# Performance work log

Measured on AMD Instinct MI355X. Metric: run time of the kernel, lower is better.

Reference implementation:

```python
import jax, jax.numpy as jnp
import numpy as np

B, S, H = 2, 1024, 2048
E_ROUTED = 8
E = E_ROUTED + 1          # +1 unconditional expert
I_MOE = 1408
I_SHARED = 5632
TOP_K = 2
UNCOND_LABEL = 1000
EPS = 1e-12


def setup_inputs() -> dict:
    key = jax.random.key(0)
    ks = jax.random.split(key, 9)
    hidden_states = jax.random.normal(ks[0], (B, S, H), dtype=jnp.float32)
    labels = jax.random.randint(ks[1], (B,), 0, 1001)
    labels = labels.at[0].set(UNCOND_LABEL)  # ensure uncond path is exercised
    cluster_centers = 0.02 * jax.random.normal(ks[2], (E_ROUTED, H), dtype=jnp.float32)
    sc = 0.02
    Wg = sc * jax.random.normal(ks[3], (E, H, I_MOE), dtype=jnp.float32)
    Wu = sc * jax.random.normal(ks[4], (E, H, I_MOE), dtype=jnp.float32)
    Wd = sc * jax.random.normal(ks[5], (E, I_MOE, H), dtype=jnp.float32)
    Wg_s = sc * jax.random.normal(ks[6], (H, I_SHARED), dtype=jnp.float32)
    Wu_s = sc * jax.random.normal(ks[7], (H, I_SHARED), dtype=jnp.float32)
    Wd_s = sc * jax.random.normal(ks[8], (I_SHARED, H), dtype=jnp.float32)
    return {"hidden_states": hidden_states, "labels": labels,
            "cluster_centers": cluster_centers,
            "Wg": Wg, "Wu": Wu, "Wd": Wd,
            "Wg_s": Wg_s, "Wu_s": Wu_s, "Wd_s": Wd_s}


def _l2norm(x):
    return x / jnp.sqrt(jnp.sum(x * x, axis=-1, keepdims=True) + EPS)


def reference(hidden_states, labels, cluster_centers, Wg, Wu, Wd, Wg_s, Wu_s, Wd_s):
    b, s, h = hidden_states.shape
    x = hidden_states.reshape(-1, h)                       # [T, H]
    flat_labels = jnp.repeat(labels, s)                     # [T]
    uncond = flat_labels == UNCOND_LABEL                    # [T]

    # cosine-sim router over routed experts
    cos = _l2norm(x) @ _l2norm(cluster_centers).T           # [T, E_routed]
    probs = jax.nn.softmax(cos, axis=-1)
    top_v, top_i = jax.lax.top_k(probs, TOP_K)              # [T, K]

    # uncond tokens: weight 1.0 in slot 0, all slots -> uncond expert (E-1)
    uncond_w = jnp.concatenate(
        [jnp.ones((1,), jnp.float32), jnp.zeros((TOP_K - 1,), jnp.float32)])
    weights = jnp.where(uncond[:, None], uncond_w[None, :], top_v)   # [T, K]
    indices = jnp.where(uncond[:, None], E - 1, top_i)               # [T, K]

    # combine weights per (token, expert): sum of slot weights hitting expert e
    onehot = (indices[:, :, None] == jnp.arange(E)[None, None, :])   # [T, K, E]
    cw = jnp.sum(weights[:, :, None] * onehot, axis=1)               # [T, E]

    # grouped expert MLPs (dense over experts; zero combine weight masks out)
    g = jnp.einsum('th,ehi->tei', x, Wg)
    u = jnp.einsum('th,ehi->tei', x, Wu)
    eo = jnp.einsum('tei,eih->teh', jax.nn.silu(g) * u, Wd)          # [T, E, H]
    out = jnp.einsum('teh,te->th', eo, cw)                           # [T, H]

    # shared expert on all tokens
    shared = (jax.nn.silu(x @ Wg_s) * (x @ Wu_s)) @ Wd_s             # [T, H]

    return (out + shared).reshape(b, s, h)
```

## Files before the change

### kernel.cpp

```cpp
#include <hip/hip_runtime.h>
#include <hip/hip_bf16.h>
#include <stdint.h>

#define T_TOK 2048
#define H_DIM 2048
#define S_SEQ 1024
#define NE_ROUTED 8
#define NE 9
#define IMOE 1408
#define ISHARED 5632
#define UNCOND_LBL 1000

typedef short bf16x8 __attribute__((ext_vector_type(8)));
typedef float f32x4 __attribute__((ext_vector_type(4)));

__device__ __forceinline__ unsigned short f2bf(float f) {
  union { float f; unsigned int u; } v; v.f = f;
  unsigned int u = v.u;
  return (unsigned short)((u + 0x7fffu + ((u >> 16) & 1u)) >> 16);
}

__device__ __forceinline__ void gl16(const void* g, void* l) {
  __builtin_amdgcn_global_load_lds(
      (const __attribute__((address_space(1))) unsigned int*)g,
      (__attribute__((address_space(3))) unsigned int*)l, 16, 0, 0);
}


__device__ __forceinline__ void transpose_body(
    const float* __restrict__ src, unsigned short* __restrict__ dst,
    int K, int N, int e, int kt, int n0, int t, float* tile ) {
  int NS = N >> 4, KT = K >> 5;
  const float* sp0 = src + (size_t)e * K * N + (size_t)kt * 32 * N + n0;
  int kr = t >> 3, nc = (t & 7) << 3;
  const float* sp = sp0 + (size_t)kr * N + nc;
  float4 a = *(const float4*)sp;
  float4 b = *(const float4*)(sp + 4);
  *(float4*)&tile[kr * 72 + nc] = a;
  *(float4*)&tile[kr * 72 + nc + 4] = b;
  __syncthreads();
  int nsl = t >> 6, up = t & 63;
  int ul = up ^ ((up >> 3) & 7);
  int rn = ul >> 2, fq = ul & 3;
  int nl = (nsl << 4) + rn;
  unsigned int pk[4];
#pragma unroll
  for (int j = 0; j < 4; j++) {
    float f0 = tile[(fq * 8 + 2 * j) * 72 + nl];
    float f1 = tile[(fq * 8 + 2 * j + 1) * 72 + nl];
    pk[j] = (unsigned)f2bf(f0) | ((unsigned)f2bf(f1) << 16);
  }
  size_t ns = (size_t)e * NS + (n0 >> 4) + nsl;
  unsigned short* dp = dst + (ns * KT + kt) * 512 + up * 8;
  *(uint4*)dp = make_uint4(pk[0], pk[1], pk[2], pk[3]);
}

__global__ __launch_bounds__(256) void prepass(
    const float* __restrict__ x, const int* __restrict__ labels,
    const float* __restrict__ cc,
    const float* __restrict__ Wg, const float* __restrict__ Wu,
    const float* __restrict__ Wd, const float* __restrict__ Wgs,
    const float* __restrict__ Wus, const float* __restrict__ Wds,
    unsigned short* __restrict__ xbf,
    int* __restrict__ counts, int* __restrict__ toklist, float* __restrict__ wts,
    unsigned short* __restrict__ WgT, unsigned short* __restrict__ WuT,
    unsigned short* __restrict__ WdT, unsigned short* __restrict__ WgsT,
    unsigned short* __restrict__ WusT, unsigned short* __restrict__ WdsT) {
  __shared__ float tile[32 * 72];
  int blk = blockIdx.x;
  int tid = threadIdx.x;

  if (blk < 4096) {
    int i = (blk * 256 + tid) * 4;
    float4 v = *(const float4*)(x + i);
    uint2 pk;
    pk.x = (unsigned)f2bf(v.x) | ((unsigned)f2bf(v.y) << 16);
    pk.y = (unsigned)f2bf(v.z) | ((unsigned)f2bf(v.w) << 16);
    *(uint2*)(xbf + i) = pk;
    return;
  }
  if (blk < 4608) {
    int t = ((blk - 4096) * 256 + tid) >> 6;
    int lane = tid & 63;
    const float* xp = x + (size_t)t * H_DIM;
    float xx = 0.f;
    float d[NE_ROUTED], cn[NE_ROUTED];
#pragma unroll
    for (int e = 0; e < NE_ROUTED; e++) { d[e] = 0.f; cn[e] = 0.f; }
    for (int h = lane; h < H_DIM; h += 64) {
      float xv = xp[h];
      xx += xv * xv;
#pragma unroll
      for (int e = 0; e < NE_ROUTED; e++) {
        float cv = cc[e * H_DIM + h];
        d[e] += xv * cv;
        cn[e] += cv * cv;
      }
    }
#pragma unroll
    for (int off = 32; off > 0; off >>= 1) {
      xx += __shfl_xor(xx, off);
#pragma unroll
      for (int e = 0; e < NE_ROUTED; e++) {
        d[e] += __shfl_xor(d[e], off);
        cn[e] += __shfl_xor(cn[e], off);
      }
    }
    if (lane == 0) {
      int lab = labels[t / S_SEQ];
      if (lab == UNCOND_LBL) {
        int r = atomicAdd(&counts[NE - 1], 1);
        toklist[(NE - 1) * T_TOK + r] = t;
        wts[(NE - 1) * T_TOK + r] = 1.0f;
      } else {
        float xn = sqrtf(xx + 1e-12f);
        float cosv[NE_ROUTED];
        float mx = -1e30f;
#pragma unroll
        for (int e = 0; e < NE_ROUTED; e++) {
          cosv[e] = d[e] / (xn * sqrtf(cn[e] + 1e-12f));
          mx = fmaxf(mx, cosv[e]);
        }
        float p[NE_ROUTED];
        float s = 0.f;
#pragma unroll
        for (int e = 0; e < NE_ROUTED; e++) { p[e] = __expf(cosv[e] - mx); s += p[e]; }
        int i1 = 0;
#pragma unroll
        for (int e = 1; e < NE_ROUTED; e++) if (p[e] > p[i1]) i1 = e;
        int i2 = (i1 == 0) ? 1 : 0;
#pragma unroll
        for (int e = 0; e < NE_ROUTED; e++) if (e != i2 && e != i1 && p[e] > p[i2]) i2 = e;
        int r1 = atomicAdd(&counts[i1], 1);
        toklist[i1 * T_TOK + r1] = t;
        wts[i1 * T_TOK + r1] = p[i1] / s;
        int r2 = atomicAdd(&counts[i2], 1);
        toklist[i2 * T_TOK + r2] = t;
        wts[i2 * T_TOK + r2] = p[i2] / s;
      }
    }
    return;
  }
  int lid = blk - 4608;
  if (lid < 12672) {
    int e = lid / 1408, r = lid % 1408;
    int kt = r / 22, n0 = (r % 22) << 6;
    transpose_body(Wg, WgT, H_DIM, IMOE, e, kt, n0, tid, tile);
  } else if (lid < 25344) {
    int r0 = lid - 12672;
    int e = r0 / 1408, r = r0 % 1408;
    int kt = r / 22, n0 = (r % 22) << 6;
    transpose_body(Wu, WuT, H_DIM, IMOE, e, kt, n0, tid, tile);
  } else if (lid < 38016) {
    int r0 = lid - 25344;
    int e = r0 / 1408, r = r0 % 1408;
    int kt = r / 32, n0 = (r % 32) << 6;
    transpose_body(Wd, WdT, IMOE, H_DIM, e, kt, n0, tid, tile);
  } else if (lid < 43648) {
    int r = lid - 38016;
    int kt = r / 88, n0 = (r % 88) << 6;
    transpose_body(Wgs, WgsT, H_DIM, ISHARED, 0, kt, n0, tid, tile);
  } else if (lid < 49280) {
    int r = lid - 43648;
    int kt = r / 88, n0 = (r % 88) << 6;
    transpose_body(Wus, WusT, H_DIM, ISHARED, 0, kt, n0, tid, tile);
  } else {
    int r = lid - 49280;
    int kt = r / 32, n0 = (r % 32) << 6;
    transpose_body(Wds, WdsT, ISHARED, H_DIM, 0, kt, n0, tid, tile);
  }
}

__device__ __forceinline__ bool up_desc(const int* counts, int d,
                                        bool* sh, int* e, int* nt, int* mt) {
  int mtm[NE];
  int nv = 352;
#pragma unroll
  for (int k = 0; k < NE; k++) {
    int c = counts[k];
    int m = (c + 255) >> 8; if (m > 8) m = 8;
    mtm[k] = m;
    nv += m * 11;
  }
  int q = nv >> 3, r = nv & 7;
  int x = d & 7, j = d >> 3;
  int cap = q + (x < r ? 1 : 0);
  if (j >= cap) return false;
  int idx = (x < r ? x * (q + 1) : r * (q + 1) + (x - r) * q) + j;
  if (idx < 352) {
    *sh = true; *e = 0; *nt = idx >> 3; *mt = idx & 7;
    return true;
  }
  idx -= 352;
#pragma unroll
  for (int k = 0; k < NE; k++) {
    int n = mtm[k] * 11;
    if (idx < n) {
      *sh = false; *e = k; *nt = idx / mtm[k]; *mt = idx % mtm[k];
      return true;
    }
    idx -= n;
  }
  return false;
}

__device__ __forceinline__ bool down_desc(const int* counts, int d,
                                          bool* sh, int* e, int* nt, int* mt, int* kc) {
  int x = d & 7, j = d >> 3;
  if (j < 32) {
    *sh = true; *e = 0; *nt = x; *mt = j >> 1; *kc = j & 1;
    return true;
  }
  int mtm[NE];
  int R = 0;
#pragma unroll
  for (int k = 0; k < NE; k++) {
    int c = counts[k];
    int m = (c + 127) >> 7; if (m > 16) m = 16;
    mtm[k] = m;
    R += m * 8;
  }
  int jr = j - 32;
  int q = R >> 3, r = R & 7;
  int cap = q + (x < r ? 1 : 0);
  if (jr >= cap) return false;
  int idx = (x < r ? x * (q + 1) : r * (q + 1) + (x - r) * q) + jr;
#pragma unroll
  for (int k = 0; k < NE; k++) {
    int n = mtm[k] * 8;
    if (idx < n) {
      *sh = false; *e = k; *nt = idx / mtm[k]; *mt = idx % mtm[k]; *kc = 0;
      return true;
    }
    idx -= n;
  }
  return false;
}

__global__ __launch_bounds__(1024) void up_merged(
    const unsigned short* __restrict__ X,
    const unsigned short* __restrict__ WgT, const unsigned short* __restrict__ WuT,
    const unsigned short* __restrict__ WgsT, const unsigned short* __restrict__ WusT,
    unsigned short* __restrict__ HhT, unsigned short* __restrict__ HsT,
    const int* __restrict__ toklist, const int* __restrict__ counts) {
  const int KT = 64;
  bool sh; int e, nt, mt;
  if (!up_desc(counts, blockIdx.x, &sh, &e, &nt, &mt)) return;

  int cnt = sh ? T_TOK : counts[e];
  int m0 = mt * 256;
  if (m0 >= cnt) return;
  int n0 = nt * 128;
  int NS = sh ? (ISHARED >> 4) : (IMOE >> 4);
  int KTO = sh ? (ISHARED >> 5) : (IMOE >> 5);
  unsigned short* Hout = sh ? HsT : HhT;
  size_t hb = sh ? 0 : (size_t)e * (T_TOK >> 4);

  __shared__ unsigned short As[4][8192];
  __shared__ unsigned short Bgs[4][4096];
  __shared__ unsigned short Bus[4][4096];

  int tid = threadIdx.x, lane = tid & 63, wid = tid >> 6;
  int wm = wid >> 2, wn = wid & 3;
  int fr = lane & 15, fq = lane >> 4;

  int v = lane ^ ((lane >> 3) & 7);
  int rr = m0 + wid * 16 + (v >> 2);
  if (rr >= cnt) rr = cnt - 1;
  int tok = sh ? rr : toklist[e * T_TOK + rr];
  const unsigned short* aptr = X + (size_t)tok * H_DIM + ((v & 3) << 3);

  size_t nsg = (sh ? 0 : (size_t)e * NS) + (n0 >> 4) + (wid & 7);
  const unsigned short* bsrc =
      ((wid >> 3) ? (sh ? WusT : WuT) : (sh ? WgsT : WgT)) + nsg * KT * 512 + lane * 8;
  unsigned short* bdstBase = (wid >> 3) ? &Bus[0][0] : &Bgs[0][0];

  int fo = fr * 4 + fq;
  fo = (fo ^ ((fo >> 3) & 7)) * 8;

  f32x4 zero = {0.f, 0.f, 0.f, 0.f};
  f32x4 accg[4][2], accu[4][2];
#pragma unroll
  for (int i = 0; i < 4; i++)
#pragma unroll
    for (int jj = 0; jj < 2; jj++) { accg[i][jj] = zero; accu[i][jj] = zero; }

  auto stageA = [&](int b, int t) {
    gl16(aptr + (size_t)t * 32, &As[b][wid * 512]);
  };
  auto stageB = [&](int b, int t) {
    gl16(bsrc + (size_t)t * 512, bdstBase + b * 4096 + (wid & 7) * 512);
  };

  stageA(0, 0); stageB(0, 0);
  stageA(1, 1); stageB(1, 1);
  stageA(2, 2); stageB(2, 2);
  asm volatile("s_waitcnt vmcnt(4)" ::: "memory");
  __builtin_amdgcn_s_barrier();

  for (int t = 0; t < KT; ++t) {
    int b = t & 3;
    bf16x8 af[4], bgf[2];
#pragma unroll
    for (int mi = 0; mi < 4; mi++)
      af[mi] = *(const bf16x8*)&As[b][(wm * 4 + mi) * 512 + fo];
#pragma unroll
    for (int ni = 0; ni < 2; ni++)
      bgf[ni] = *(const bf16x8*)&Bgs[b][(wn * 2 + ni) * 512 + fo];
    if (t + 3 < KT) stageA((t + 3) & 3, t + 3);
    __builtin_amdgcn_s_setprio(1);
#pragma unroll
    for (int mi = 0; mi < 4; mi++)
#pragma unroll
      for (int ni = 0; ni < 2; ni++)
        accg[mi][ni] = __builtin_amdgcn_mfma_f32_16x16x32_bf16(af[mi], bgf[ni], accg[mi][ni], 0, 0, 0);
    __builtin_amdgcn_s_setprio(0);
    bf16x8 buf2[2];
#pragma unroll
    for (int ni = 0; ni < 2; ni++)
      buf2[ni] = *(const bf16x8*)&Bus[b][(wn * 2 + ni) * 512 + fo];
    if (t + 3 < KT) stageB((t + 3) & 3, t + 3);
    __builtin_amdgcn_s_setprio(1);
#pragma unroll
    for (int mi = 0; mi < 4; mi++)
#pragma unroll
      for (int ni = 0; ni < 2; ni++)
        accu[mi][ni] = __builtin_amdgcn_mfma_f32_16x16x32_bf16(af[mi], buf2[ni], accu[mi][ni], 0, 0, 0);
    __builtin_amdgcn_s_setprio(0);
    if (t + 3 < KT) {
      asm volatile("s_waitcnt vmcnt(4)" ::: "memory");
      __builtin_amdgcn_s_barrier();
    } else if (t + 2 < KT) {
      asm volatile("s_waitcnt vmcnt(2)" ::: "memory");
      __builtin_amdgcn_s_barrier();
    } else if (t + 1 < KT) {
      asm volatile("s_waitcnt vmcnt(0)" ::: "memory");
      __builtin_amdgcn_s_barrier();
    }
  }

#pragma unroll
  for (int mi = 0; mi < 4; mi++) {
    int rb = m0 + wm * 64 + mi * 16;
    if (rb >= cnt) continue;
    int ms = rb >> 4;
#pragma unroll
    for (int ni = 0; ni < 2; ni++) {
      int col = n0 + wn * 32 + ni * 16 + fr;
      int kto = col >> 5;
      int c3 = (col >> 3) & 3;
      int jcol = col & 7;
      size_t base = ((hb + ms) * (size_t)KTO + kto) * 512 + jcol;
#pragma unroll
      for (int jj = 0; jj < 4; jj++) {
        int row = rb + fq * 4 + jj;
        if (row < cnt) {
          float g = accg[mi][ni][jj];
          float u = accu[mi][ni][jj];
          float h = g / (1.f + __expf(-g)) * u;
          int ul = (fq * 4 + jj) * 4 + c3;
          int ph = ul ^ ((ul >> 3) & 7);
          Hout[base + ph * 8] = f2bf(h);
        }
      }
    }
  }
}

__global__ __launch_bounds__(512, 4) void down_merged(
    const unsigned short* __restrict__ HhT, const unsigned short* __restrict__ HsT,
    const unsigned short* __restrict__ WdT, const unsigned short* __restrict__ WdsT,
    float* __restrict__ Out,
    const int* __restrict__ toklist, const float* __restrict__ wts,
    const int* __restrict__ counts) {
  bool sh; int e, nt, mt, kc;
  if (!down_desc(counts, blockIdx.x, &sh, &e, &nt, &mt, &kc)) return;

  int cnt = sh ? T_TOK : counts[e];
  int m0 = mt * 128;
  if (m0 >= cnt) return;
  int n0 = nt * 256;
  int KTfull = sh ? (ISHARED >> 5) : (IMOE >> 5);
  int KT = sh ? 88 : 44;
  int koff = kc * 88;
  const int NS = H_DIM >> 4;

  __shared__ unsigned short As[3][4096];
  __shared__ unsigned short Bs[3][8192];

  int tid = threadIdx.x, lane = tid & 63, wid = tid >> 6;
  int wm = wid >> 2, wn = wid & 3;
  int fr = lane & 15, fq = lane >> 4;

  const unsigned short* Hin = sh ? HsT : HhT;
  size_t mbase = sh ? 0 : (size_t)e * (T_TOK >> 4);
  size_t ms = mbase + (m0 >> 4) + wid;
  const unsigned short* ap = Hin + ms * (size_t)KTfull * 512 + lane * 8;
  const unsigned short* WdBase = sh ? WdsT : WdT;
  size_t nsbase = (sh ? 0 : (size_t)e * NS) + (n0 >> 4);
  const unsigned short* bp0 = WdBase + (nsbase + wid * 2) * (size_t)KTfull * 512 + lane * 8;
  const unsigned short* bp1 = WdBase + (nsbase + wid * 2 + 1) * (size_t)KTfull * 512 + lane * 8;

  int fo = fr * 4 + fq;
  fo = (fo ^ ((fo >> 3) & 7)) * 8;

  f32x4 zero = {0.f, 0.f, 0.f, 0.f};
  f32x4 acc[4][4];
#pragma unroll
  for (int i = 0; i < 4; i++)
#pragma unroll
    for (int jj = 0; jj < 4; jj++) acc[i][jj] = zero;

  auto stage = [&](int b, int t) {
    gl16(ap + (size_t)(koff + t) * 512, &As[b][wid * 512]);
    gl16(bp0 + (size_t)(koff + t) * 512, &Bs[b][(wid * 2) * 512]);
    gl16(bp1 + (size_t)(koff + t) * 512, &Bs[b][(wid * 2 + 1) * 512]);
  };

  stage(0, 0);
  stage(1, 1);
  asm volatile("s_waitcnt vmcnt(3)" ::: "memory");
  __builtin_amdgcn_s_barrier();

  for (int t = 0; t < KT; ++t) {
    int b = t % 3;
    bf16x8 af[4], bf[4];
#pragma unroll
    for (int mi = 0; mi < 4; mi++)
      af[mi] = *(const bf16x8*)&As[b][(wm * 4 + mi) * 512 + fo];
#pragma unroll
    for (int ni = 0; ni < 4; ni++)
      bf[ni] = *(const bf16x8*)&Bs[b][(wn * 4 + ni) * 512 + fo];
    if (t + 2 < KT) {
      int nb = t + 2; nb %= 3;
      stage(nb, t + 2);
    }
    __builtin_amdgcn_s_setprio(1);
#pragma unroll
    for (int mi = 0; mi < 4; mi++)
#pragma unroll
      for (int ni = 0; ni < 4; ni++)
        acc[mi][ni] = __builtin_amdgcn_mfma_f32_16x16x32_bf16(af[mi], bf[ni], acc[mi][ni], 0, 0, 0);
    __builtin_amdgcn_s_setprio(0);
    if (t + 2 < KT) {
      asm volatile("s_waitcnt vmcnt(3)" ::: "memory");
      __builtin_amdgcn_s_barrier();
    } else if (t + 1 < KT) {
      asm volatile("s_waitcnt vmcnt(0)" ::: "memory");
      __builtin_amdgcn_s_barrier();
    }
  }

  int rbase = m0 + wm * 64;
  int cbase = n0 + wn * 64;
#pragma unroll
  for (int mi = 0; mi < 4; mi++)
#pragma unroll
    for (int ni = 0; ni < 4; ni++) {
      int col = cbase + ni * 16 + fr;
#pragma unroll
      for (int jj = 0; jj < 4; jj++) {
        int row = rbase + mi * 16 + fq * 4 + jj;
        if (row < cnt) {
          float vv = acc[mi][ni][jj];
          int tk;
          float wgt;
          if (sh) { tk = row; wgt = 1.0f; }
          else { tk = toklist[e * T_TOK + row]; wgt = wts[e * T_TOK + row]; }
          atomicAdd(&Out[(size_t)tk * H_DIM + col], wgt * vv);
        }
      }
    }
}

extern "C" void kernel_launch(void* const* d_in, const int* in_sizes, int n_in,
                              void* d_out, int out_size, void* d_ws, size_t ws_size,
                              hipStream_t stream) {
  const float* x = (const float*)d_in[0];
  const int* labels = (const int*)d_in[1];
  const float* cc = (const float*)d_in[2];
  const float* Wg = (const float*)d_in[3];
  const float* Wu = (const float*)d_in[4];
  const float* Wd = (const float*)d_in[5];
  const float* Wgs = (const float*)d_in[6];
  const float* Wus = (const float*)d_in[7];
  const float* Wds = (const float*)d_in[8];
  float* out = (float*)d_out;

  uint8_t* p = (uint8_t*)d_ws;
  int* counts = (int*)p;            p += 256;
  int* toklist = (int*)p;           p += (size_t)NE * T_TOK * 4;
  float* wts = (float*)p;           p += (size_t)NE * T_TOK * 4;
  unsigned short* xbf = (unsigned short*)p;  p += (size_t)T_TOK * H_DIM * 2;
  unsigned short* WgT = (unsigned short*)p;  p += (size_t)NE * H_DIM * IMOE * 2;
  unsigned short* WuT = (unsigned short*)p;  p += (size_t)NE * H_DIM * IMOE * 2;
  unsigned short* WdT = (unsigned short*)p;  p += (size_t)NE * IMOE * H_DIM * 2;
  unsigned short* WgsT = (unsigned short*)p; p += (size_t)H_DIM * ISHARED * 2;
  unsigned short* WusT = (unsigned short*)p; p += (size_t)H_DIM * ISHARED * 2;
  unsigned short* WdsT = (unsigned short*)p; p += (size_t)ISHARED * H_DIM * 2;
  unsigned short* HhT = (unsigned short*)p;  p += (size_t)NE * T_TOK * IMOE * 2;
  unsigned short* HsT = (unsigned short*)p;  p += (size_t)T_TOK * ISHARED * 2;
  size_t need = (size_t)(p - (uint8_t*)d_ws);
  if (ws_size < need) return;

  hipMemsetAsync(d_ws, 0, 64, stream);
  hipMemsetAsync(d_out, 0, (size_t)out_size * 4, stream);

  prepass<<<59520, 256, 0, stream>>>(x, labels, cc, Wg, Wu, Wd, Wgs, Wus, Wds,
                                     xbf, counts, toklist, wts,
                                     WgT, WuT, WdT, WgsT, WusT, WdsT);

  up_merged<<<1144, 1024, 0, stream>>>(xbf, WgT, WuT, WgsT, WusT, HhT, HsT,
                                       toklist, counts);

  down_merged<<<1408, 512, 0, stream>>>(HhT, HsT, WdT, WdsT, out,
                                        toklist, wts, counts);
}
```

Baseline: 420.6 us.

## Halve up-projection M tile to 128 with 512-thread blocks and triple buffering

```diff
diff --git a/kernel.cpp b/kernel.cpp
--- a/kernel.cpp
+++ b/kernel.cpp
@@ -174,11 +174,11 @@
 __device__ __forceinline__ bool up_desc(const int* counts, int d,
                                         bool* sh, int* e, int* nt, int* mt) {
   int mtm[NE];
-  int nv = 352;
+  int nv = 704;
 #pragma unroll
   for (int k = 0; k < NE; k++) {
     int c = counts[k];
-    int m = (c + 255) >> 8; if (m > 8) m = 8;
+    int m = (c + 127) >> 7; if (m > 16) m = 16;
     mtm[k] = m;
     nv += m * 11;
   }
@@ -187,11 +187,11 @@
   int cap = q + (x < r ? 1 : 0);
   if (j >= cap) return false;
   int idx = (x < r ? x * (q + 1) : r * (q + 1) + (x - r) * q) + j;
-  if (idx < 352) {
-    *sh = true; *e = 0; *nt = idx >> 3; *mt = idx & 7;
+  if (idx < 704) {
+    *sh = true; *e = 0; *nt = idx >> 4; *mt = idx & 15;
     return true;
   }
-  idx -= 352;
+  idx -= 704;
 #pragma unroll
   for (int k = 0; k < NE; k++) {
     int n = mtm[k] * 11;
@@ -237,7 +237,7 @@
   return false;
 }
 
-__global__ __launch_bounds__(1024) void up_merged(
+__global__ __launch_bounds__(512, 4) void up_merged(
     const unsigned short* __restrict__ X,
     const unsigned short* __restrict__ WgT, const unsigned short* __restrict__ WuT,
     const unsigned short* __restrict__ WgsT, const unsigned short* __restrict__ WusT,
@@ -248,7 +248,7 @@
   if (!up_desc(counts, blockIdx.x, &sh, &e, &nt, &mt)) return;
 
   int cnt = sh ? T_TOK : counts[e];
-  int m0 = mt * 256;
+  int m0 = mt * 128;
   if (m0 >= cnt) return;
   int n0 = nt * 128;
   int NS = sh ? (ISHARED >> 4) : (IMOE >> 4);
@@ -256,9 +256,9 @@
   unsigned short* Hout = sh ? HsT : HhT;
   size_t hb = sh ? 0 : (size_t)e * (T_TOK >> 4);
 
-  __shared__ unsigned short As[4][8192];
-  __shared__ unsigned short Bgs[4][4096];
-  __shared__ unsigned short Bus[4][4096];
+  __shared__ unsigned short As[3][4096];
+  __shared__ unsigned short Bgs[3][4096];
+  __shared__ unsigned short Bus[3][4096];
 
   int tid = threadIdx.x, lane = tid & 63, wid = tid >> 6;
   int wm = wid >> 2, wn = wid & 3;
@@ -270,10 +270,9 @@
   int tok = sh ? rr : toklist[e * T_TOK + rr];
   const unsigned short* aptr = X + (size_t)tok * H_DIM + ((v & 3) << 3);
 
-  size_t nsg = (sh ? 0 : (size_t)e * NS) + (n0 >> 4) + (wid & 7);
-  const unsigned short* bsrc =
-      ((wid >> 3) ? (sh ? WusT : WuT) : (sh ? WgsT : WgT)) + nsg * KT * 512 + lane * 8;
-  unsigned short* bdstBase = (wid >> 3) ? &Bus[0][0] : &Bgs[0][0];
+  size_t nsg = (sh ? 0 : (size_t)e * NS) + (n0 >> 4) + wid;
+  const unsigned short* bgp = (sh ? WgsT : WgT) + nsg * KT * 512 + lane * 8;
+  const unsigned short* bup = (sh ? WusT : WuT) + nsg * KT * 512 + lane * 8;
 
   int fo = fr * 4 + fq;
   fo = (fo ^ ((fo >> 3) & 7)) * 8;
@@ -285,53 +284,43 @@
 #pragma unroll
     for (int jj = 0; jj < 2; jj++) { accg[i][jj] = zero; accu[i][jj] = zero; }
 
-  auto stageA = [&](int b, int t) {
+  auto stage = [&](int b, int t) {
     gl16(aptr + (size_t)t * 32, &As[b][wid * 512]);
+    gl16(bgp + (size_t)t * 512, &Bgs[b][wid * 512]);
+    gl16(bup + (size_t)t * 512, &Bus[b][wid * 512]);
   };
-  auto stageB = [&](int b, int t) {
-    gl16(bsrc + (size_t)t * 512, bdstBase + b * 4096 + (wid & 7) * 512);
-  };
-
-  stageA(0, 0); stageB(0, 0);
-  stageA(1, 1); stageB(1, 1);
-  stageA(2, 2); stageB(2, 2);
-  asm volatile("s_waitcnt vmcnt(4)" ::: "memory");
+
+  stage(0, 0);
+  stage(1, 1);
+  asm volatile("s_waitcnt vmcnt(3)" ::: "memory");
   __builtin_amdgcn_s_barrier();
 
   for (int t = 0; t < KT; ++t) {
-    int b = t & 3;
-    bf16x8 af[4], bgf[2];
+    int b = t % 3;
+    bf16x8 af[4], bgf[2], buf2[2];
 #pragma unroll
     for (int mi = 0; mi < 4; mi++)
       af[mi] = *(const bf16x8*)&As[b][(wm * 4 + mi) * 512 + fo];
 #pragma unroll
-    for (int ni = 0; ni < 2; ni++)
+    for (int ni = 0; ni < 2; ni++) {
       bgf[ni] = *(const bf16x8*)&Bgs[b][(wn * 2 + ni) * 512 + fo];
-    if (t + 3 < KT) stageA((t + 3) & 3, t + 3);
+      buf2[ni] = *(const bf16x8*)&Bus[b][(wn * 2 + ni) * 512 + fo];
+    }
+    if (t + 2 < KT) {
+      int nb = t + 2; nb %= 3;
+      stage(nb, t + 2);
+    }
     __builtin_amdgcn_s_setprio(1);
 #pragma unroll
     for (int mi = 0; mi < 4; mi++)
 #pragma unroll
-      for (int ni = 0; ni < 2; ni++)
+      for (int ni = 0; ni < 2; ni++) {
         accg[mi][ni] = __builtin_amdgcn_mfma_f32_16x16x32_bf16(af[mi], bgf[ni], accg[mi][ni], 0, 0, 0);
+        accu[mi][ni] = __builtin_amdgcn_mfma_f32_16x16x32_bf16(af[mi], buf2[ni], accu[mi][ni], 0, 0, 0);
+      }
     __builtin_amdgcn_s_setprio(0);
-    bf16x8 buf2[2];
-#pragma unroll
-    for (int ni = 0; ni < 2; ni++)
-      buf2[ni] = *(const bf16x8*)&Bus[b][(wn * 2 + ni) * 512 + fo];
-    if (t + 3 < KT) stageB((t + 3) & 3, t + 3);
-    __builtin_amdgcn_s_setprio(1);
-#pragma unroll
-    for (int mi = 0; mi < 4; mi++)
-#pragma unroll
-      for (int ni = 0; ni < 2; ni++)
-        accu[mi][ni] = __builtin_amdgcn_mfma_f32_16x16x32_bf16(af[mi], buf2[ni], accu[mi][ni], 0, 0, 0);
-    __builtin_amdgcn_s_setprio(0);
-    if (t + 3 < KT) {
-      asm volatile("s_waitcnt vmcnt(4)" ::: "memory");
-      __builtin_amdgcn_s_barrier();
-    } else if (t + 2 < KT) {
-      asm volatile("s_waitcnt vmcnt(2)" ::: "memory");
+    if (t + 2 < KT) {
+      asm volatile("s_waitcnt vmcnt(3)" ::: "memory");
       __builtin_amdgcn_s_barrier();
     } else if (t + 1 < KT) {
       asm volatile("s_waitcnt vmcnt(0)" ::: "memory");
@@ -510,8 +499,8 @@
                                      xbf, counts, toklist, wts,
                                      WgT, WuT, WdT, WgsT, WusT, WdsT);
 
-  up_merged<<<1144, 1024, 0, stream>>>(xbf, WgT, WuT, WgsT, WusT, HhT, HsT,
-                                       toklist, counts);
+  up_merged<<<2288, 512, 0, stream>>>(xbf, WgT, WuT, WgsT, WusT, HhT, HsT,
+                                      toklist, counts);
 
   down_merged<<<1408, 512, 0, stream>>>(HhT, HsT, WdT, WdsT, out,
                                         toklist, wts, counts);
```

After: 399.2 us. -5.1%, faster.
